# Kernel optimization log

Measured on AMD Instinct MI355X. Metric: run time of the kernel, lower is better.

## Reference

```python
import math
import jax, jax.numpy as jnp
import numpy as np

VOCAB, D, H, L, DFF, MAXLEN, PAD = 32000, 512, 8, 6, 2048, 5000, 0
DK = D // H
EPS = 1e-5


def _positional_encoding(max_len, d_model):
    pos = np.arange(max_len, dtype=np.float32)[:, None]
    div = np.exp(np.arange(0, d_model, 2, dtype=np.float32) * (-math.log(10000.0) / d_model))
    pe = np.zeros((max_len, d_model), dtype=np.float32)
    pe[:, 0::2] = np.sin(pos * div)
    pe[:, 1::2] = np.cos(pos * div)
    return jnp.asarray(pe)


def setup_inputs() -> dict:
    key = jax.random.key(0)
    ks = jax.random.split(key, 16)
    B, S = 2, 2048
    src = jax.random.randint(ks[0], (B, S), 0, VOCAB)
    emb = jax.random.normal(ks[1], (VOCAB, D), jnp.float32) * (D ** -0.5)
    emb = emb.at[PAD].set(0.0)  # padding_idx row zeroed
    pe = _positional_encoding(MAXLEN, D)
    s = 0.02
    WQ = jax.random.normal(ks[2], (L, D, D), jnp.float32) * s
    WK = jax.random.normal(ks[3], (L, D, D), jnp.float32) * s
    WV = jax.random.normal(ks[4], (L, D, D), jnp.float32) * s
    WO = jax.random.normal(ks[5], (L, D, D), jnp.float32) * s
    W1 = jax.random.normal(ks[6], (L, D, DFF), jnp.float32) * s
    b1 = jnp.zeros((L, DFF), jnp.float32)
    W2 = jax.random.normal(ks[7], (L, DFF, D), jnp.float32) * s
    b2 = jnp.zeros((L, D), jnp.float32)
    ln1_s = jnp.ones((L, D), jnp.float32); ln1_b = jnp.zeros((L, D), jnp.float32)
    ln2_s = jnp.ones((L, D), jnp.float32); ln2_b = jnp.zeros((L, D), jnp.float32)
    fn_s = jnp.ones((D,), jnp.float32); fn_b = jnp.zeros((D,), jnp.float32)
    return dict(src=src, emb=emb, pe=pe, WQ=WQ, WK=WK, WV=WV, WO=WO,
                W1=W1, b1=b1, W2=W2, b2=b2, ln1_s=ln1_s, ln1_b=ln1_b,
                ln2_s=ln2_s, ln2_b=ln2_b, fn_s=fn_s, fn_b=fn_b)


def _layernorm(x, scale, bias):
    mu = jnp.mean(x, axis=-1, keepdims=True)
    var = jnp.mean(jnp.square(x - mu), axis=-1, keepdims=True)
    return (x - mu) * jax.lax.rsqrt(var + EPS) * scale + bias


def _encoder_forward(src, emb, pe, WQ, WK, WV, WO, W1, b1, W2, b2,
                     ln1_s, ln1_b, ln2_s, ln2_b, fn_s, fn_b):
    B, S = src.shape
    key_mask = (src != PAD)[:, None, None, :]  # [B,1,1,S] padding mask
    x = emb[src] * math.sqrt(D) + pe[:S]        # [B,S,D] (dropout=eval/off)
    for l in range(L):
        # --- pre-LN self-attention ---
        h = _layernorm(x, ln1_s[l], ln1_b[l])
        q = (h @ WQ[l]).reshape(B, S, H, DK).transpose(0, 2, 1, 3)
        k = (h @ WK[l]).reshape(B, S, H, DK).transpose(0, 2, 1, 3)
        v = (h @ WV[l]).reshape(B, S, H, DK).transpose(0, 2, 1, 3)
        scores = jnp.einsum('bhqd,bhkd->bhqk', q, k) / math.sqrt(DK)
        scores = jnp.where(key_mask, scores, -jnp.inf)
        w = jax.nn.softmax(scores, axis=-1)
        w = jnp.nan_to_num(w, nan=0.0)
        attn = jnp.einsum('bhqk,bhkd->bhqd', w, v)
        attn = attn.transpose(0, 2, 1, 3).reshape(B, S, D) @ WO[l]
        x = x + attn
        # --- pre-LN FFN ---
        h = _layernorm(x, ln2_s[l], ln2_b[l])
        h = jax.nn.relu(h @ W1[l] + b1[l]) @ W2[l] + b2[l]
        x = x + h
    return _layernorm(x, fn_s, fn_b)


def reference(src, emb, pe, WQ, WK, WV, WO, W1, b1, W2, b2,
              ln1_s, ln1_b, ln2_s, ln2_b, fn_s, fn_b):
    return _encoder_forward(src, emb, pe, WQ, WK, WV, WO, W1, b1, W2, b2,
                            ln1_s, ln1_b, ln2_s, ln2_b, fn_s, fn_b)
```

## Files before the change

kernel.cpp:

```cpp
#include <hip/hip_runtime.h>


typedef _Float16 f16;
typedef _Float16 f16x8 __attribute__((ext_vector_type(8)));
typedef _Float16 f16x4 __attribute__((ext_vector_type(4)));
typedef float    f32x4 __attribute__((ext_vector_type(4)));

#define MFMA16(a, b, c) __builtin_amdgcn_mfma_f32_16x16x32_f16((a), (b), (c), 0, 0, 0)
#define GLOAD_LDS16(GP, LP)                                        \
  __builtin_amdgcn_global_load_lds(                                \
      (const __attribute__((address_space(1))) void*)(GP),         \
      (__attribute__((address_space(3))) void*)(LP), 16, 0, 0)

__device__ inline float fast_exp2(float x) {
#if __has_builtin(__builtin_amdgcn_exp2f)
  return __builtin_amdgcn_exp2f(x);
#else
  return exp2f(x);
#endif
}

static constexpr int Dm  = 512;
static constexpr int Sx  = 2048;
static constexpr int NTOK = 4096;
static constexpr int DFFm = 2048;
static constexpr int Lc  = 6;

__global__ __launch_bounds__(256) void transpose_cvt(
    const float* __restrict__ in, f16* __restrict__ out, int R, int C)
{
  __shared__ float t[32][33];
  const int z = blockIdx.z;
  const float* src = in + (size_t)z * R * C;
  f16* dst = out + (size_t)z * R * C;
  const int r0 = blockIdx.y * 32, c0 = blockIdx.x * 32;
  const int tx = threadIdx.x, ty = threadIdx.y;
  #pragma unroll
  for (int i = 0; i < 4; i++)
    t[ty + i * 8][tx] = src[(size_t)(r0 + ty + i * 8) * C + c0 + tx];
  __syncthreads();
  #pragma unroll
  for (int i = 0; i < 4; i++)
    dst[(size_t)(c0 + ty + i * 8) * R + r0 + tx] = (f16)t[tx][ty + i * 8];
}

__global__ __launch_bounds__(256) void embed_k(
    const int* __restrict__ src, const float* __restrict__ emb,
    const float* __restrict__ pe, float* __restrict__ x)
{
  const int gid = blockIdx.x * 256 + threadIdx.x;
  const int token = gid >> 6;
  const int d0 = (gid & 63) << 3;
  const int s = token & (Sx - 1);
  const int tk = src[token];
  const float* e = emb + (size_t)tk * Dm + d0;
  const float* p = pe + (size_t)s * Dm + d0;
  float* o = x + (size_t)token * Dm + d0;
  const float SC = 22.627416997969522f;
  #pragma unroll
  for (int j = 0; j < 8; j++) o[j] = e[j] * SC + p[j];
}

__global__ __launch_bounds__(256) void mask_k(
    const int* __restrict__ src, float* __restrict__ mb)
{
  const int i = blockIdx.x * 256 + threadIdx.x;
  mb[i] = (src[i] != 0) ? 0.f : -3.0e38f;
}

template <typename OUT>
__global__ __launch_bounds__(256) void ln_k(
    const float* __restrict__ x, const float* __restrict__ sc,
    const float* __restrict__ bi, OUT* __restrict__ out)
{
  const int row = blockIdx.x * 4 + (threadIdx.x >> 6);
  const int l = threadIdx.x & 63;
  const float* px = x + (size_t)row * Dm + l * 8;
  float v[8];
  *(float4*)&v[0] = *(const float4*)px;
  *(float4*)&v[4] = *(const float4*)(px + 4);
  float s = 0.f;
  #pragma unroll
  for (int j = 0; j < 8; j++) s += v[j];
  #pragma unroll
  for (int m = 1; m < 64; m <<= 1) s += __shfl_xor(s, m);
  const float mu = s * (1.0f / 512.0f);
  float qv = 0.f;
  #pragma unroll
  for (int j = 0; j < 8; j++) { float d = v[j] - mu; qv += d * d; }
  #pragma unroll
  for (int m = 1; m < 64; m <<= 1) qv += __shfl_xor(qv, m);
  const float inv = rsqrtf(qv * (1.0f / 512.0f) + 1e-5f);
  float scv[8], biv[8];
  *(float4*)&scv[0] = *(const float4*)(sc + l * 8);
  *(float4*)&scv[4] = *(const float4*)(sc + l * 8 + 4);
  *(float4*)&biv[0] = *(const float4*)(bi + l * 8);
  *(float4*)&biv[4] = *(const float4*)(bi + l * 8 + 4);
  if constexpr (sizeof(OUT) == 2) {
    f16x8 o;
    #pragma unroll
    for (int j = 0; j < 8; j++) o[j] = (f16)((v[j] - mu) * inv * scv[j] + biv[j]);
    *(f16x8*)((f16*)out + (size_t)row * Dm + l * 8) = o;
  } else {
    float o[8];
    #pragma unroll
    for (int j = 0; j < 8; j++) o[j] = (v[j] - mu) * inv * scv[j] + biv[j];
    float* po = (float*)out + (size_t)row * Dm + l * 8;
    *(float4*)po = *(float4*)&o[0];
    *(float4*)(po + 4) = *(float4*)&o[4];
  }
}

template <int BN, int MODE, int N, int K>
__global__ __launch_bounds__(256) void gemm_k(
    const f16* __restrict__ A,
    const f16* __restrict__ B0, const f16* __restrict__ B1, const f16* __restrict__ B2,
    f16* __restrict__ O0, f16* __restrict__ O1, f16* __restrict__ O2,
    float* __restrict__ xio, const float* __restrict__ bias)
{
  constexpr int BM = 128;
  constexpr int NF = BN / 32;
  constexpr int NBM = NTOK / BM;
  constexpr int NBN = N / BN;
  constexpr int NZ = (MODE == 0) ? 3 : 1;
  constexpr int NB = NBM * NBN * NZ;
  __shared__ f16 lsA[2][BM * 64];
  __shared__ f16 lsB[2][BN * 64];
  const int tid = threadIdx.x;
  const int l = tid & 63, w = tid >> 6;
  const int lr = l & 15, lh = l >> 4;
  const int wm = w >> 1, wn = w & 1;
  const int bid = blockIdx.x;
  const int nid = (bid & 7) * (NB / 8) + (bid >> 3);
  const int z = nid / (NBM * NBN);
  const int rr = nid % (NBM * NBN);
  const int bm = rr / NBN, bn = rr % NBN;
  const f16* Bt = (z == 0) ? B0 : ((z == 1) ? B1 : B2);
  f16* Oz = (z == 0) ? O0 : O1;

  constexpr int ACH = (BM * 64) / (256 * 8);
  constexpr int BCH = (BN * 64) / (256 * 8);
  const size_t rowA0 = (size_t)bm * BM;
  const size_t rowB0 = (size_t)bn * BN;

  auto stage = [&](int kt, int pb) {
    #pragma unroll
    for (int i = 0; i < ACH; i++) {
      int c = i * 256 + tid;
      GLOAD_LDS16(A + (rowA0 + (c >> 3)) * K + kt * 64 + (c & 7) * 8, &lsA[pb][c * 8]);
    }
    #pragma unroll
    for (int i = 0; i < BCH; i++) {
      int c = i * 256 + tid;
      GLOAD_LDS16(Bt + (rowB0 + (c >> 3)) * K + kt * 64 + (c & 7) * 8, &lsB[pb][c * 8]);
    }
  };

  f32x4 acc[4][NF] = {};
  stage(0, 0);
  constexpr int NT = K >> 6;
  for (int kt = 0; kt < NT; ++kt) {
    const int cur = kt & 1;
    __syncthreads();
    if (kt + 1 < NT) stage(kt + 1, cur ^ 1);
    #pragma unroll
    for (int s = 0; s < 2; s++) {
      f16x8 af[4], bf[NF];
      #pragma unroll
      for (int mf = 0; mf < 4; mf++)
        af[mf] = *(const f16x8*)(&lsA[cur][(wm * 64 + mf * 16 + lr) * 64 + s * 32 + lh * 8]);
      #pragma unroll
      for (int nf = 0; nf < NF; nf++)
        bf[nf] = *(const f16x8*)(&lsB[cur][(wn * (BN / 2) + nf * 16 + lr) * 64 + s * 32 + lh * 8]);
      #pragma unroll
      for (int mf = 0; mf < 4; mf++)
        #pragma unroll
        for (int nf = 0; nf < NF; nf++)
          acc[mf][nf] = MFMA16(af[mf], bf[nf], acc[mf][nf]);
    }
  }

  #pragma unroll
  for (int mf = 0; mf < 4; mf++) {
    #pragma unroll
    for (int nf = 0; nf < NF; nf++) {
      const int token = bm * BM + wm * 64 + mf * 16 + lh * 4;
      const int ch = bn * BN + wn * (BN / 2) + nf * 16 + lr;
      if constexpr (MODE == 0) {
        if (z == 2) {
          f16x4 o;
          #pragma unroll
          for (int r = 0; r < 4; r++) o[r] = (f16)acc[mf][nf][r];
          const int bb = token >> 11, ss = token & (Sx - 1);
          const int scol = (ss & ~31) | (((ss >> 2) & 3) << 3) | (((ss >> 4) & 1) << 2);
          *(f16x4*)(O2 + ((size_t)((bb << 3) + (ch >> 6)) * 64 + (ch & 63)) * Sx + scol) = o;
        } else {
          #pragma unroll
          for (int r = 0; r < 4; r++)
            Oz[(size_t)(token + r) * N + ch] = (f16)acc[mf][nf][r];
        }
      } else {
        #pragma unroll
        for (int r = 0; r < 4; r++) {
          float v = acc[mf][nf][r];
          size_t idx = (size_t)(token + r) * N + ch;
          if constexpr (MODE == 1) {
            xio[idx] += v;
          } else if constexpr (MODE == 2) {
            v += bias[ch];
            O0[idx] = (f16)fmaxf(v, 0.f);
          } else {
            xio[idx] += v + bias[ch];
          }
        }
      }
    }
  }
}

__global__ __launch_bounds__(512) void attn_k(
    const f16* __restrict__ q, const f16* __restrict__ kk,
    const f16* __restrict__ vt, const float* __restrict__ maskb,
    f16* __restrict__ out)
{
  __shared__ f16 lsK[2][2][64 * 64];
  __shared__ f16 lsV[2][2][64 * 64];
  const int tid = threadIdx.x;
  const int l = tid & 63, w = tid >> 6;
  const int lr = l & 15, lh = l >> 4;
  const int grp = w >> 2;
  const int t256 = tid & 255;
  const int bid = blockIdx.x;
  const int nid = ((bid & 7) << 6) + (bid >> 3);
  const int bh = nid >> 5;
  const int qt = nid & 31;
  const int b = bh >> 3, h = bh & 7;

  const _Float16 QS = (_Float16)0.18033688f;
  f16x8 qf[2];
  #pragma unroll
  for (int s = 0; s < 2; s++) {
    size_t row = (size_t)(b * Sx + qt * 64 + (w & 3) * 16 + lr);
    f16x8 t = *(const f16x8*)(q + row * Dm + h * 64 + s * 32 + lh * 8);
    qf[s] = t * QS;
  }

  const f16x8 ones = {(f16)1, (f16)1, (f16)1, (f16)1,
                      (f16)1, (f16)1, (f16)1, (f16)1};
  f32x4 oacc[4] = {};
  f32x4 sumacc = {};
  float mrun = -1e30f;

  auto stage = [&](int t, int pb) {
    #pragma unroll
    for (int i = 0; i < 2; i++) {
      int c = i * 256 + t256, r = c >> 3, g = c & 7, gs = g ^ (r & 7);
      GLOAD_LDS16(kk + (size_t)(b * Sx + t * 64 + r) * Dm + h * 64 + gs * 8,
                  &lsK[grp][pb][c * 8]);
      GLOAD_LDS16(vt + (size_t)(bh * 64 + r) * Sx + t * 64 + gs * 8,
                  &lsV[grp][pb][c * 8]);
    }
  };
  stage(grp * 16, 0);

  for (int i = 0; i < 16; ++i) {
    const int t = grp * 16 + i;
    const int cur = i & 1;
    __syncthreads();
    if (i < 15) stage(t + 1, cur ^ 1);

    f32x4 sacc[4];
    #pragma unroll
    for (int kf = 0; kf < 4; kf++)
      sacc[kf] = *(const f32x4*)(maskb + b * Sx + t * 64 + kf * 16 + lh * 4);
    __builtin_amdgcn_s_setprio(1);
    #pragma unroll
    for (int s = 0; s < 2; s++) {
      const int gk = (s * 4 + lh) ^ (lr & 7);
      #pragma unroll
      for (int kf = 0; kf < 4; kf++) {
        f16x8 a = *(const f16x8*)(&lsK[grp][cur][(kf * 16 + lr) * 64 + gk * 8]);
        sacc[kf] = MFMA16(a, qf[s], sacc[kf]);
      }
    }
    __builtin_amdgcn_s_setprio(0);

    float pmax;
    {
      float t0 = fmaxf(fmaxf(sacc[0][0], sacc[0][1]), sacc[0][2]);
      float t1 = fmaxf(fmaxf(sacc[0][3], sacc[1][0]), sacc[1][1]);
      float t2 = fmaxf(fmaxf(sacc[1][2], sacc[1][3]), sacc[2][0]);
      float t3 = fmaxf(fmaxf(sacc[2][1], sacc[2][2]), sacc[2][3]);
      float t4 = fmaxf(fmaxf(sacc[3][0], sacc[3][1]), sacc[3][2]);
      float u0 = fmaxf(fmaxf(t0, t1), sacc[3][3]);
      float u1 = fmaxf(fmaxf(t2, t3), t4);
      pmax = fmaxf(u0, u1);
    }
    pmax = fmaxf(pmax, __shfl_xor(pmax, 16));
    pmax = fmaxf(pmax, __shfl_xor(pmax, 32));
    if (!__all(pmax - mrun <= 8.0f)) {
      const float mnew = fmaxf(mrun, pmax);
      const float rs = fast_exp2(mrun - mnew);
      sumacc *= rs;
      #pragma unroll
      for (int mf = 0; mf < 4; mf++) oacc[mf] *= rs;
      mrun = mnew;
    }
    #pragma unroll
    for (int kf = 0; kf < 4; kf++)
      #pragma unroll
      for (int r = 0; r < 4; r++)
        sacc[kf][r] = fast_exp2(sacc[kf][r] - mrun);
    f16x8 pa[2];
    #pragma unroll
    for (int s = 0; s < 2; s++)
      #pragma unroll
      for (int jj = 0; jj < 8; jj++)
        pa[s][jj] = (f16)sacc[2 * s + (jj >> 2)][jj & 3];
    sumacc = MFMA16(ones, pa[0], sumacc);
    sumacc = MFMA16(ones, pa[1], sumacc);

    __builtin_amdgcn_s_setprio(1);
    #pragma unroll
    for (int s = 0; s < 2; s++) {
      const int gv = (4 * s + lh) ^ (lr & 7);
      #pragma unroll
      for (int mf = 0; mf < 4; mf++) {
        f16x8 vv = *(const f16x8*)(&lsV[grp][cur][(mf * 16 + lr) * 64 + gv * 8]);
        oacc[mf] = MFMA16(vv, pa[s], oacc[mf]);
      }
    }
    __builtin_amdgcn_s_setprio(0);
  }

  const float lrun = sumacc[0];
  __syncthreads();
  float* sO  = (float*)&lsK[0][0][0];
  float* sML = (float*)&lsV[0][0][0];
  const int wl = (w & 3) * 64 + l;
  if (grp == 1) {
    #pragma unroll
    for (int mf = 0; mf < 4; mf++)
      #pragma unroll
      for (int r = 0; r < 4; r++) sO[wl * 16 + mf * 4 + r] = oacc[mf][r];
    sML[wl * 2] = mrun;
    sML[wl * 2 + 1] = lrun;
  }
  __syncthreads();
  if (grp == 0) {
    const float m1 = sML[wl * 2], l1 = sML[wl * 2 + 1];
    const float mm = fmaxf(mrun, m1);
    const float s0 = fast_exp2(mrun - mm), s1 = fast_exp2(m1 - mm);
    const float inv = 1.f / (lrun * s0 + l1 * s1);
    size_t row = (size_t)(b * Sx + qt * 64 + (w & 3) * 16 + lr);
    #pragma unroll
    for (int mf = 0; mf < 4; mf++) {
      f16x4 o;
      #pragma unroll
      for (int r = 0; r < 4; r++)
        o[r] = (f16)((oacc[mf][r] * s0 + sO[wl * 16 + mf * 4 + r] * s1) * inv);
      *(f16x4*)(out + row * Dm + h * 64 + mf * 16 + lh * 4) = o;
    }
  }
}

extern "C" void kernel_launch(void* const* d_in, const int* in_sizes, int n_in,
                              void* d_out, int out_size, void* d_ws, size_t ws_size,
                              hipStream_t stream)
{
  (void)in_sizes; (void)n_in; (void)out_size; (void)ws_size;
  const int*   src  = (const int*)d_in[0];
  const float* emb  = (const float*)d_in[1];
  const float* pe   = (const float*)d_in[2];
  const float* WQ   = (const float*)d_in[3];
  const float* WK   = (const float*)d_in[4];
  const float* WV   = (const float*)d_in[5];
  const float* WO   = (const float*)d_in[6];
  const float* W1   = (const float*)d_in[7];
  const float* b1   = (const float*)d_in[8];
  const float* W2   = (const float*)d_in[9];
  const float* b2   = (const float*)d_in[10];
  const float* ln1s = (const float*)d_in[11];
  const float* ln1b = (const float*)d_in[12];
  const float* ln2s = (const float*)d_in[13];
  const float* ln2b = (const float*)d_in[14];
  const float* fns  = (const float*)d_in[15];
  const float* fnb  = (const float*)d_in[16];

  char* ws = (char*)d_ws;
  const size_t DD = (size_t)Dm * Dm;
  const size_t DF = (size_t)Dm * DFFm;
  f16* wtQ = (f16*)(ws);
  f16* wtK = wtQ + Lc * DD;
  f16* wtV = wtK + Lc * DD;
  f16* wtO = wtV + Lc * DD;
  f16* wt1 = wtO + Lc * DD;
  f16* wt2 = wt1 + Lc * DF;
  float* x  = (float*)(wt2 + Lc * DF);
  f16* hbuf = (f16*)(x + (size_t)NTOK * Dm);
  f16* qb   = hbuf + (size_t)NTOK * Dm;
  f16* kb   = qb + (size_t)NTOK * Dm;
  f16* vtb  = kb + (size_t)NTOK * Dm;
  f16* attn = vtb + (size_t)NTOK * Dm;
  f16* ff   = attn + (size_t)NTOK * Dm;
  float* maskb = (float*)(ff + (size_t)NTOK * DFFm);

  const dim3 tb(32, 8);
  transpose_cvt<<<dim3(16, 16, Lc), tb, 0, stream>>>(WQ, wtQ, Dm, Dm);
  transpose_cvt<<<dim3(16, 16, Lc), tb, 0, stream>>>(WK, wtK, Dm, Dm);
  transpose_cvt<<<dim3(16, 16, Lc), tb, 0, stream>>>(WV, wtV, Dm, Dm);
  transpose_cvt<<<dim3(16, 16, Lc), tb, 0, stream>>>(WO, wtO, Dm, Dm);
  transpose_cvt<<<dim3(64, 16, Lc), tb, 0, stream>>>(W1, wt1, Dm, DFFm);
  transpose_cvt<<<dim3(16, 64, Lc), tb, 0, stream>>>(W2, wt2, DFFm, Dm);

  embed_k<<<1024, 256, 0, stream>>>(src, emb, pe, x);
  mask_k<<<16, 256, 0, stream>>>(src, maskb);

  for (int l = 0; l < Lc; l++) {
    const f16* wq = wtQ + (size_t)l * DD;
    const f16* wk = wtK + (size_t)l * DD;
    const f16* wv = wtV + (size_t)l * DD;
    const f16* wo = wtO + (size_t)l * DD;
    const f16* w1 = wt1 + (size_t)l * DF;
    const f16* w2 = wt2 + (size_t)l * DF;

    ln_k<f16><<<1024, 256, 0, stream>>>(x, ln1s + l * Dm, ln1b + l * Dm, hbuf);
    gemm_k<64, 0, 512, 512><<<768, 256, 0, stream>>>(
        hbuf, wq, wk, wv, qb, kb, vtb, nullptr, nullptr);
    attn_k<<<512, 512, 0, stream>>>(qb, kb, vtb, maskb, attn);
    gemm_k<32, 1, 512, 512><<<512, 256, 0, stream>>>(
        attn, wo, wo, wo, nullptr, nullptr, nullptr, x, nullptr);
    ln_k<f16><<<1024, 256, 0, stream>>>(x, ln2s + l * Dm, ln2b + l * Dm, hbuf);
    gemm_k<128, 2, 2048, 512><<<512, 256, 0, stream>>>(
        hbuf, w1, w1, w1, ff, ff, ff, nullptr, b1 + (size_t)l * DFFm);
    gemm_k<32, 3, 512, 2048><<<512, 256, 0, stream>>>(
        ff, w2, w2, w2, nullptr, nullptr, nullptr, x, b2 + (size_t)l * Dm);
  }

  ln_k<float><<<1024, 256, 0, stream>>>(x, fns, fnb, (float*)d_out);
}
```

Before: 734.9 us.

## Fuse QKV weights into one GEMM, add split-K atomics, swizzle LDS tiles

Packs the Q, K and V transposed weights into one 1536-wide matrix so the QKV projection runs as a single GEMM with BN=128 tiles and routes each output column to Q, K or V by channel. The WO and W2 GEMMs switch to BN=64 with split-K of 2, accumulating into the residual with float atomics and adding the bias only from the first split. Each LDS tile is XOR-swizzled per row to cut bank conflicts on the fragment reads. Atomics make the summation order nondeterministic and add contention on the residual buffer.

```diff
diff --git a/kernel.cpp b/kernel.cpp
--- a/kernel.cpp
+++ b/kernel.cpp
@@ -27,12 +27,13 @@
 static constexpr int Lc  = 6;
 
 __global__ __launch_bounds__(256) void transpose_cvt(
-    const float* __restrict__ in, f16* __restrict__ out, int R, int C)
+    const float* __restrict__ in, f16* __restrict__ out, int R, int C,
+    size_t zsi, size_t zso)
 {
   __shared__ float t[32][33];
   const int z = blockIdx.z;
-  const float* src = in + (size_t)z * R * C;
-  f16* dst = out + (size_t)z * R * C;
+  const float* src = in + (size_t)z * zsi;
+  f16* dst = out + (size_t)z * zso;
   const int r0 = blockIdx.y * 32, c0 = blockIdx.x * 32;
   const int tx = threadIdx.x, ty = threadIdx.y;
   #pragma unroll
@@ -111,10 +112,9 @@
   }
 }
 
-template <int BN, int MODE, int N, int K>
+template <int BN, int MODE, int N, int K, int SK>
 __global__ __launch_bounds__(256) void gemm_k(
-    const f16* __restrict__ A,
-    const f16* __restrict__ B0, const f16* __restrict__ B1, const f16* __restrict__ B2,
+    const f16* __restrict__ A, const f16* __restrict__ Bt,
     f16* __restrict__ O0, f16* __restrict__ O1, f16* __restrict__ O2,
     float* __restrict__ xio, const float* __restrict__ bias)
 {
@@ -122,8 +122,7 @@
   constexpr int NF = BN / 32;
   constexpr int NBM = NTOK / BM;
   constexpr int NBN = N / BN;
-  constexpr int NZ = (MODE == 0) ? 3 : 1;
-  constexpr int NB = NBM * NBN * NZ;
+  constexpr int NB = NBM * NBN * SK;
   __shared__ f16 lsA[2][BM * 64];
   __shared__ f16 lsB[2][BN * 64];
   const int tid = threadIdx.x;
@@ -132,46 +131,46 @@
   const int wm = w >> 1, wn = w & 1;
   const int bid = blockIdx.x;
   const int nid = (bid & 7) * (NB / 8) + (bid >> 3);
-  const int z = nid / (NBM * NBN);
+  const int ks = nid / (NBM * NBN);
   const int rr = nid % (NBM * NBN);
   const int bm = rr / NBN, bn = rr % NBN;
-  const f16* Bt = (z == 0) ? B0 : ((z == 1) ? B1 : B2);
-  f16* Oz = (z == 0) ? O0 : O1;
 
   constexpr int ACH = (BM * 64) / (256 * 8);
   constexpr int BCH = (BN * 64) / (256 * 8);
   const size_t rowA0 = (size_t)bm * BM;
   const size_t rowB0 = (size_t)bn * BN;
+  const int k0 = ks * (K / SK);
 
   auto stage = [&](int kt, int pb) {
     #pragma unroll
     for (int i = 0; i < ACH; i++) {
-      int c = i * 256 + tid;
-      GLOAD_LDS16(A + (rowA0 + (c >> 3)) * K + kt * 64 + (c & 7) * 8, &lsA[pb][c * 8]);
+      int c = i * 256 + tid, r = c >> 3, g = c & 7, gs = g ^ (r & 7);
+      GLOAD_LDS16(A + (rowA0 + r) * K + k0 + kt * 64 + gs * 8, &lsA[pb][c * 8]);
     }
     #pragma unroll
     for (int i = 0; i < BCH; i++) {
-      int c = i * 256 + tid;
-      GLOAD_LDS16(Bt + (rowB0 + (c >> 3)) * K + kt * 64 + (c & 7) * 8, &lsB[pb][c * 8]);
+      int c = i * 256 + tid, r = c >> 3, g = c & 7, gs = g ^ (r & 7);
+      GLOAD_LDS16(Bt + (rowB0 + r) * K + k0 + kt * 64 + gs * 8, &lsB[pb][c * 8]);
     }
   };
 
   f32x4 acc[4][NF] = {};
   stage(0, 0);
-  constexpr int NT = K >> 6;
+  constexpr int NT = (K / SK) >> 6;
   for (int kt = 0; kt < NT; ++kt) {
     const int cur = kt & 1;
     __syncthreads();
     if (kt + 1 < NT) stage(kt + 1, cur ^ 1);
     #pragma unroll
     for (int s = 0; s < 2; s++) {
+      const int gg = (s * 4 + lh) ^ (lr & 7);
       f16x8 af[4], bf[NF];
       #pragma unroll
       for (int mf = 0; mf < 4; mf++)
-        af[mf] = *(const f16x8*)(&lsA[cur][(wm * 64 + mf * 16 + lr) * 64 + s * 32 + lh * 8]);
+        af[mf] = *(const f16x8*)(&lsA[cur][(wm * 64 + mf * 16 + lr) * 64 + gg * 8]);
       #pragma unroll
       for (int nf = 0; nf < NF; nf++)
-        bf[nf] = *(const f16x8*)(&lsB[cur][(wn * (BN / 2) + nf * 16 + lr) * 64 + s * 32 + lh * 8]);
+        bf[nf] = *(const f16x8*)(&lsB[cur][(wn * (BN / 2) + nf * 16 + lr) * 64 + gg * 8]);
       #pragma unroll
       for (int mf = 0; mf < 4; mf++)
         #pragma unroll
@@ -187,17 +186,20 @@
       const int token = bm * BM + wm * 64 + mf * 16 + lh * 4;
       const int ch = bn * BN + wn * (BN / 2) + nf * 16 + lr;
       if constexpr (MODE == 0) {
-        if (z == 2) {
+        const int part = ch >> 9;
+        const int pch = ch & 511;
+        if (part == 2) {
           f16x4 o;
           #pragma unroll
           for (int r = 0; r < 4; r++) o[r] = (f16)acc[mf][nf][r];
           const int bb = token >> 11, ss = token & (Sx - 1);
           const int scol = (ss & ~31) | (((ss >> 2) & 3) << 3) | (((ss >> 4) & 1) << 2);
-          *(f16x4*)(O2 + ((size_t)((bb << 3) + (ch >> 6)) * 64 + (ch & 63)) * Sx + scol) = o;
+          *(f16x4*)(O2 + ((size_t)((bb << 3) + (pch >> 6)) * 64 + (pch & 63)) * Sx + scol) = o;
         } else {
+          f16* Oz = (part == 0) ? O0 : O1;
           #pragma unroll
           for (int r = 0; r < 4; r++)
-            Oz[(size_t)(token + r) * N + ch] = (f16)acc[mf][nf][r];
+            Oz[(size_t)(token + r) * Dm + pch] = (f16)acc[mf][nf][r];
         }
       } else {
         #pragma unroll
@@ -205,12 +207,15 @@
           float v = acc[mf][nf][r];
           size_t idx = (size_t)(token + r) * N + ch;
           if constexpr (MODE == 1) {
-            xio[idx] += v;
+            if constexpr (SK > 1) unsafeAtomicAdd(&xio[idx], v);
+            else                  xio[idx] += v;
           } else if constexpr (MODE == 2) {
             v += bias[ch];
             O0[idx] = (f16)fmaxf(v, 0.f);
           } else {
-            xio[idx] += v + bias[ch];
+            if (ks == 0) v += bias[ch];
+            if constexpr (SK > 1) unsafeAtomicAdd(&xio[idx], v);
+            else                  xio[idx] += v;
           }
         }
       }
@@ -389,13 +394,12 @@
 
   char* ws = (char*)d_ws;
   const size_t DD = (size_t)Dm * Dm;
+  const size_t DQKV = (size_t)1536 * Dm;
   const size_t DF = (size_t)Dm * DFFm;
-  f16* wtQ = (f16*)(ws);
-  f16* wtK = wtQ + Lc * DD;
-  f16* wtV = wtK + Lc * DD;
-  f16* wtO = wtV + Lc * DD;
-  f16* wt1 = wtO + Lc * DD;
-  f16* wt2 = wt1 + Lc * DF;
+  f16* wqkv = (f16*)(ws);
+  f16* wtO  = wqkv + Lc * DQKV;
+  f16* wt1  = wtO + Lc * DD;
+  f16* wt2  = wt1 + Lc * DF;
   float* x  = (float*)(wt2 + Lc * DF);
   f16* hbuf = (f16*)(x + (size_t)NTOK * Dm);
   f16* qb   = hbuf + (size_t)NTOK * Dm;
@@ -406,35 +410,33 @@
   float* maskb = (float*)(ff + (size_t)NTOK * DFFm);
 
   const dim3 tb(32, 8);
-  transpose_cvt<<<dim3(16, 16, Lc), tb, 0, stream>>>(WQ, wtQ, Dm, Dm);
-  transpose_cvt<<<dim3(16, 16, Lc), tb, 0, stream>>>(WK, wtK, Dm, Dm);
-  transpose_cvt<<<dim3(16, 16, Lc), tb, 0, stream>>>(WV, wtV, Dm, Dm);
-  transpose_cvt<<<dim3(16, 16, Lc), tb, 0, stream>>>(WO, wtO, Dm, Dm);
-  transpose_cvt<<<dim3(64, 16, Lc), tb, 0, stream>>>(W1, wt1, Dm, DFFm);
-  transpose_cvt<<<dim3(16, 64, Lc), tb, 0, stream>>>(W2, wt2, DFFm, Dm);
+  transpose_cvt<<<dim3(16, 16, Lc), tb, 0, stream>>>(WQ, wqkv, Dm, Dm, DD, DQKV);
+  transpose_cvt<<<dim3(16, 16, Lc), tb, 0, stream>>>(WK, wqkv + 512 * Dm, Dm, Dm, DD, DQKV);
+  transpose_cvt<<<dim3(16, 16, Lc), tb, 0, stream>>>(WV, wqkv + 1024 * Dm, Dm, Dm, DD, DQKV);
+  transpose_cvt<<<dim3(16, 16, Lc), tb, 0, stream>>>(WO, wtO, Dm, Dm, DD, DD);
+  transpose_cvt<<<dim3(64, 16, Lc), tb, 0, stream>>>(W1, wt1, Dm, DFFm, DF, DF);
+  transpose_cvt<<<dim3(16, 64, Lc), tb, 0, stream>>>(W2, wt2, DFFm, Dm, DF, DF);
 
   embed_k<<<1024, 256, 0, stream>>>(src, emb, pe, x);
   mask_k<<<16, 256, 0, stream>>>(src, maskb);
 
   for (int l = 0; l < Lc; l++) {
-    const f16* wq = wtQ + (size_t)l * DD;
-    const f16* wk = wtK + (size_t)l * DD;
-    const f16* wv = wtV + (size_t)l * DD;
+    const f16* wqkv_l = wqkv + (size_t)l * DQKV;
     const f16* wo = wtO + (size_t)l * DD;
     const f16* w1 = wt1 + (size_t)l * DF;
     const f16* w2 = wt2 + (size_t)l * DF;
 
     ln_k<f16><<<1024, 256, 0, stream>>>(x, ln1s + l * Dm, ln1b + l * Dm, hbuf);
-    gemm_k<64, 0, 512, 512><<<768, 256, 0, stream>>>(
-        hbuf, wq, wk, wv, qb, kb, vtb, nullptr, nullptr);
+    gemm_k<128, 0, 1536, 512, 1><<<384, 256, 0, stream>>>(
+        hbuf, wqkv_l, qb, kb, vtb, nullptr, nullptr);
     attn_k<<<512, 512, 0, stream>>>(qb, kb, vtb, maskb, attn);
-    gemm_k<32, 1, 512, 512><<<512, 256, 0, stream>>>(
-        attn, wo, wo, wo, nullptr, nullptr, nullptr, x, nullptr);
+    gemm_k<64, 1, 512, 512, 2><<<512, 256, 0, stream>>>(
+        attn, wo, nullptr, nullptr, nullptr, x, nullptr);
     ln_k<f16><<<1024, 256, 0, stream>>>(x, ln2s + l * Dm, ln2b + l * Dm, hbuf);
-    gemm_k<128, 2, 2048, 512><<<512, 256, 0, stream>>>(
-        hbuf, w1, w1, w1, ff, ff, ff, nullptr, b1 + (size_t)l * DFFm);
-    gemm_k<32, 3, 512, 2048><<<512, 256, 0, stream>>>(
-        ff, w2, w2, w2, nullptr, nullptr, nullptr, x, b2 + (size_t)l * Dm);
+    gemm_k<128, 2, 2048, 512, 1><<<512, 256, 0, stream>>>(
+        hbuf, w1, ff, nullptr, nullptr, nullptr, b1 + (size_t)l * DFFm);
+    gemm_k<64, 3, 512, 2048, 2><<<512, 256, 0, stream>>>(
+        ff, w2, nullptr, nullptr, nullptr, x, b2 + (size_t)l * Dm);
   }
 
   ln_k<float><<<1024, 256, 0, stream>>>(x, fns, fnb, (float*)d_out);
```

Result: no change. 740.3 us (+0.7%).
